# Kernel optimization log

Measured on AMD Instinct MI355X. Metric: run time of the kernel, lower is better.

Reference implementation:

```python
import jax, jax.numpy as jnp
import numpy as np

N = 50000      # total nodes across batched subgraphs
E = 800000     # total edges
R = 4          # num_relations
G = 16         # number of graphs (questions) in batch
NODE_DIM = 128
QDIM = 768
RQ = 64        # reduced_qn_dim
RN = 64        # reduced_node_dim
H = 128        # hidden_dim
OUT = 64       # output_dim


def setup_inputs() -> dict:
    key = jax.random.key(0)
    ks = jax.random.split(key, 16)
    def lin(k, i, o):
        return jax.random.normal(k, (i, o), jnp.float32) / np.float32(np.sqrt(i))
    def rel(k, i, o):
        return jax.random.normal(k, (R, i, o), jnp.float32) / np.float32(np.sqrt(i))
    return {
        "x": jax.random.normal(ks[0], (N, NODE_DIM), jnp.float32),
        "edge_index": jax.random.randint(ks[1], (2, E), 0, N, dtype=jnp.int32),
        "edge_attr": jax.random.randint(ks[2], (E,), 0, R, dtype=jnp.int32),
        "batch": jnp.sort(jax.random.randint(ks[3], (N,), 0, G, dtype=jnp.int32)),
        "question_embedding": jax.random.normal(ks[4], (G, QDIM), jnp.float32),
        "qn_W": lin(ks[5], QDIM, RQ), "qn_b": jnp.zeros((RQ,), jnp.float32),
        "W0": rel(ks[6], NODE_DIM, RN), "root0": lin(ks[7], NODE_DIM, RN), "b0": jnp.zeros((RN,), jnp.float32),
        "W1": rel(ks[8], RN + RQ, H), "root1": lin(ks[9], RN + RQ, H), "b1": jnp.zeros((H,), jnp.float32),
        "W2": rel(ks[10], H, H), "root2": lin(ks[11], H, H), "b2": jnp.zeros((H,), jnp.float32),
        "W3": rel(ks[12], H, OUT), "root3": lin(ks[13], H, OUT), "b3": jnp.zeros((OUT,), jnp.float32),
    }


def rgcn_conv(x, src, dst, etype, W, root, b):
    """PyG RGCNConv: out_i = x_i @ root + b + sum_r mean_{j in N_r(i)} x_j @ W_r."""
    out = x @ root + b
    for r in range(R):
        h = x @ W[r]                                  # [N, out] transform-then-gather
        mask = (etype == r)
        msgs = jnp.where(mask[:, None], h[src], 0.0)  # [E, out]
        s = jax.ops.segment_sum(msgs, dst, num_segments=N)
        cnt = jax.ops.segment_sum(mask.astype(x.dtype), dst, num_segments=N)
        out = out + s / jnp.maximum(cnt, 1.0)[:, None]
    return out


def reference(x, edge_index, edge_attr, batch, question_embedding,
              qn_W, qn_b, W0, root0, b0, W1, root1, b1, W2, root2, b2, W3, root3, b3):
    src, dst = edge_index[0], edge_index[1]
    q = jax.nn.relu(question_embedding @ qn_W + qn_b)          # [G, RQ]
    h = jax.nn.relu(rgcn_conv(x, src, dst, edge_attr, W0, root0, b0))
    combined = jnp.concatenate([h, q[batch]], axis=1)          # [N, RN+RQ]
    h = jax.nn.relu(rgcn_conv(combined, src, dst, edge_attr, W1, root1, b1))
    h = jax.nn.relu(rgcn_conv(h, src, dst, edge_attr, W2, root2, b2))
    return rgcn_conv(h, src, dst, edge_attr, W3, root3, b3)
```

## Files before the change

### kernel.cpp

```cpp
#include <hip/hip_runtime.h>
#include <hip/hip_bf16.h>

#define NN 50000
#define EE 800000
#define GG 16
#define QD 768
#define NBUCK 196
#define EPB 4000

typedef __bf16 bf16x8 __attribute__((ext_vector_type(8)));
typedef float f32x4 __attribute__((ext_vector_type(4)));

static __device__ __forceinline__ float bflo(unsigned u) {
    union { unsigned v; float f; } c; c.v = u << 16; return c.f;
}
static __device__ __forceinline__ float bfhi(unsigned u) {
    union { unsigned v; float f; } c; c.v = u & 0xffff0000u; return c.f;
}


__global__ void qkern(const float* __restrict__ qe, const float* __restrict__ W,
                      const float* __restrict__ b, float* __restrict__ q) {
    int g = blockIdx.x, o = threadIdx.x;
    float s = b[o];
    for (int k = 0; k < QD; ++k) s = fmaf(qe[g * QD + k], W[k * 64 + o], s);
    q[g * 64 + o] = fmaxf(s, 0.f);
}

__global__ void convert_x(const float* __restrict__ x, __hip_bfloat16* __restrict__ xb, int n4) {
    int i = blockIdx.x * blockDim.x + threadIdx.x;
    if (i >= n4) return;
    float4 v = ((const float4*)x)[i];
    union { ushort4 u; __hip_bfloat16 h[4]; } o;
    o.h[0] = __float2bfloat16(v.x); o.h[1] = __float2bfloat16(v.y);
    o.h[2] = __float2bfloat16(v.z); o.h[3] = __float2bfloat16(v.w);
    ((ushort4*)xb)[i] = o.u;
}

__global__ void prep_w(const float* __restrict__ W, const float* __restrict__ root,
                       __hip_bfloat16* __restrict__ WT, int O) {
    int idx = blockIdx.x * blockDim.x + threadIdx.x;
    int total = 5 * O * 128;
    if (idx >= total) return;
    int n = idx >> 7, k = idx & 127;
    float v;
    if (n < 4 * O) { int r = n / O, o = n - r * O; v = W[((size_t)r * 128 + k) * O + o]; }
    else           { int o = n - 4 * O;            v = root[(size_t)k * O + o]; }
    WT[idx] = __float2bfloat16(v);
}


__global__ void bucket_hist(const int* __restrict__ dst, int* __restrict__ bcnt) {
    __shared__ int h[NBUCK];
    int tid = threadIdx.x;
    for (int i = tid; i < NBUCK; i += 256) h[i] = 0;
    __syncthreads();
    for (int e = blockIdx.x * 256 + tid; e < EE; e += gridDim.x * 256)
        atomicAdd(&h[dst[e] >> 8], 1);
    __syncthreads();
    for (int i = tid; i < NBUCK; i += 256) if (h[i]) atomicAdd(&bcnt[i], h[i]);
}

__global__ void bucket_scan(const int* __restrict__ bcnt, int* __restrict__ bbase,
                            int* __restrict__ bcur) {
    __shared__ int wt[4];
    int tid = threadIdx.x, lane = tid & 63, w = tid >> 6;
    int v = (tid < NBUCK) ? bcnt[tid] : 0;
    int sc = v;
#pragma unroll
    for (int off = 1; off < 64; off <<= 1) {
        int t = __shfl_up(sc, off, 64);
        if (lane >= off) sc += t;
    }
    if (lane == 63) wt[w] = sc;
    __syncthreads();
    int wbase = 0;
    for (int ww = 0; ww < w; ++ww) wbase += wt[ww];
    int excl = wbase + sc - v;
    if (tid <= NBUCK) bbase[tid] = excl;
    if (tid < NBUCK) bcur[tid] = excl;
}

__global__ __launch_bounds__(256) void bin_edges(const int* __restrict__ src,
                                                 const int* __restrict__ dst,
                                                 const int* __restrict__ et,
                                                 int* __restrict__ bcur,
                                                 unsigned* __restrict__ binned) {
    __shared__ int lcnt[NBUCK];
    __shared__ int lbase[NBUCK];
    int tid = threadIdx.x;
    int e0 = blockIdx.x * EPB, e1 = min(e0 + EPB, EE);
    for (int base = e0; base < e1; base += 2048) {
        for (int i = tid; i < NBUCK; i += 256) lcnt[i] = 0;
        __syncthreads();
        unsigned ent[8]; int bk[8], rk[8];
#pragma unroll
        for (int k = 0; k < 8; ++k) {
            int e = base + k * 256 + tid;
            if (e < e1) {
                int d = dst[e];
                bk[k] = d >> 8;
                ent[k] = ((unsigned)src[e] << 10) | ((unsigned)et[e] << 8) | (unsigned)(d & 255);
                rk[k] = atomicAdd(&lcnt[bk[k]], 1);
            } else bk[k] = -1;
        }
        __syncthreads();
        for (int i = tid; i < NBUCK; i += 256)
            lbase[i] = lcnt[i] ? atomicAdd(&bcur[i], lcnt[i]) : 0;
        __syncthreads();
#pragma unroll
        for (int k = 0; k < 8; ++k)
            if (bk[k] >= 0) binned[lbase[bk[k]] + rk[k]] = ent[k];
        __syncthreads();
    }
}

__global__ __launch_bounds__(256) void csr_fine(const int* __restrict__ bbase,
                                                const unsigned* __restrict__ binned,
                                                int* __restrict__ csr,
                                                int* __restrict__ offsets,
                                                float* __restrict__ inv4) {
    __shared__ int cnt[1024];
    __shared__ int wt[4];
    int b = blockIdx.x, tid = threadIdx.x, lane = tid & 63, w = tid >> 6;
    int seg0 = bbase[b], seg1 = bbase[b + 1];
    for (int i = tid; i < 1024; i += 256) cnt[i] = 0;
    __syncthreads();
    for (int e = seg0 + tid; e < seg1; e += 256) {
        unsigned u = binned[e];
        atomicAdd(&cnt[(u & 255) * 4 + ((u >> 8) & 3)], 1);
    }
    __syncthreads();
    int c0 = cnt[tid * 4], c1 = cnt[tid * 4 + 1], c2 = cnt[tid * 4 + 2], c3 = cnt[tid * 4 + 3];
    int s = c0 + c1 + c2 + c3;
    int sc = s;
#pragma unroll
    for (int off = 1; off < 64; off <<= 1) {
        int t = __shfl_up(sc, off, 64);
        if (lane >= off) sc += t;
    }
    if (lane == 63) wt[w] = sc;
    __syncthreads();
    int wbase = 0;
    for (int ww = 0; ww < w; ++ww) wbase += wt[ww];
    int excl = wbase + sc - s;
    cnt[tid * 4]     = excl;
    cnt[tid * 4 + 1] = excl + c0;
    cnt[tid * 4 + 2] = excl + c0 + c1;
    cnt[tid * 4 + 3] = excl + c0 + c1 + c2;
    int node = b * 256 + tid;
    if (node < NN) {
        offsets[node] = seg0 + excl;
        float4 iv;
        iv.x = 1.f / fmaxf((float)c0, 1.f);
        iv.y = 1.f / fmaxf((float)c1, 1.f);
        iv.z = 1.f / fmaxf((float)c2, 1.f);
        iv.w = 1.f / fmaxf((float)c3, 1.f);
        ((float4*)inv4)[node] = iv;
    }
    if (b == NBUCK - 1 && tid == 0) offsets[NN] = EE;
    __syncthreads();
    for (int e = seg0 + tid; e < seg1; e += 256) {
        unsigned u = binned[e];
        int r = atomicAdd(&cnt[(u & 255) * 4 + ((u >> 8) & 3)], 1);
        csr[seg0 + r] = (int)(((u >> 10) << 2) | ((u >> 8) & 3));
    }
}


template <int O>
__global__ __launch_bounds__(256) void dense_mm(const __hip_bfloat16* __restrict__ X,
                                                const __hip_bfloat16* __restrict__ WT,
                                                __hip_bfloat16* __restrict__ hall_b,
                                                float* __restrict__ hroot) {
    __shared__ char tilebuf[4][4096];
    int wave = threadIdx.x >> 6;
    int lane = threadIdx.x & 63;
    int quad = lane >> 4, l15 = lane & 15;
    int cg = blockIdx.x;
    int slot = (O == 64) ? cg : (cg >> 1);
    int colbase = (O == 128 && (cg & 1)) ? 64 : 0;
    const __bf16* Xs = (const __bf16*)X;
    const __bf16* Ws = (const __bf16*)WT;

    bf16x8 b[4][4];
#pragma unroll
    for (int kk = 0; kk < 4; ++kk)
#pragma unroll
        for (int t = 0; t < 4; ++t)
            b[kk][t] = *(const bf16x8*)(Ws + (size_t)(cg * 64 + t * 16 + l15) * 128 + kk * 32 + quad * 8);

    int tile0 = blockIdx.y * 32 + wave * 8;
    for (int i = 0; i < 8; ++i) {
        int tile = tile0 + i;
        if (tile >= NN / 16) break;
        int m0 = tile * 16;

        bf16x8 a[4];
#pragma unroll
        for (int kk = 0; kk < 4; ++kk)
            a[kk] = *(const bf16x8*)(Xs + (size_t)(m0 + l15) * 128 + kk * 32 + quad * 8);

        f32x4 acc[4] = {f32x4{0,0,0,0}, f32x4{0,0,0,0}, f32x4{0,0,0,0}, f32x4{0,0,0,0}};
#pragma unroll
        for (int kk = 0; kk < 4; ++kk)
#pragma unroll
            for (int t = 0; t < 4; ++t)
                acc[t] = __builtin_amdgcn_mfma_f32_16x16x32_bf16(a[kk], b[kk][t], acc[t], 0, 0, 0);

        if (slot == 4) {
            float* tp = (float*)tilebuf[wave];
#pragma unroll
            for (int t = 0; t < 4; ++t)
#pragma unroll
                for (int reg = 0; reg < 4; ++reg)
                    tp[(quad * 4 + reg) * 64 + t * 16 + l15] = acc[t][reg];
#pragma unroll
            for (int p = 0; p < 4; ++p) {
                int c = p * 64 + lane;
                int row = c >> 4, col0 = (c & 15) * 4;
                *(f32x4*)&hroot[(size_t)(m0 + row) * O + colbase + col0] =
                    ((const f32x4*)tp)[c];
            }
        } else {
            __hip_bfloat16* tp = (__hip_bfloat16*)tilebuf[wave];
#pragma unroll
            for (int t = 0; t < 4; ++t)
#pragma unroll
                for (int reg = 0; reg < 4; ++reg)
                    tp[(quad * 4 + reg) * 64 + t * 16 + l15] = __float2bfloat16(acc[t][reg]);
#pragma unroll
            for (int p = 0; p < 2; ++p) {
                int c = p * 64 + lane;
                int row = c >> 3, col0 = (c & 7) * 8;
                *(uint4*)&hall_b[((size_t)(m0 + row) * 4 + slot) * O + colbase + col0] =
                    ((const uint4*)tp)[c];
            }
        }
    }
}


template <int O, int MODE>
__global__ __launch_bounds__(256) void aggregate(const __hip_bfloat16* __restrict__ hall_b,
                                                 const float* __restrict__ hroot,
                                                 const int* __restrict__ offsets,
                                                 const int* __restrict__ csr,
                                                 const float* __restrict__ inv4,
                                                 const float* __restrict__ bias,
                                                 const float* __restrict__ q,
                                                 const int* __restrict__ batch,
                                                 __hip_bfloat16* __restrict__ xnext,
                                                 float* __restrict__ out) {
    int node = blockIdx.x * 4 + (threadIdx.x >> 6);
    int lane = threadIdx.x & 63;
    int e0 = offsets[node], e1 = offsets[node + 1];
    float4 iv = ((const float4*)inv4)[node];
    float acc0 = 0.f, acc1 = 0.f;
    const char* hb = (const char*)hall_b;
    for (int base = e0; base < e1; base += 64) {
        int e = base + lane;
        int packed = (e < e1) ? csr[e] : 0;
        int m = min(64, e1 - base);
        int j = 0;
        for (; j + 4 <= m; j += 4) {
            int p0 = __builtin_amdgcn_readlane(packed, j);
            int p1 = __builtin_amdgcn_readlane(packed, j + 1);
            int p2 = __builtin_amdgcn_readlane(packed, j + 2);
            int p3 = __builtin_amdgcn_readlane(packed, j + 3);
            int r0 = p0 & 3, r1 = p1 & 3, r2 = p2 & 3, r3 = p3 & 3;
            float w0 = (r0 == 0) ? iv.x : (r0 == 1) ? iv.y : (r0 == 2) ? iv.z : iv.w;
            float w1 = (r1 == 0) ? iv.x : (r1 == 1) ? iv.y : (r1 == 2) ? iv.z : iv.w;
            float w2 = (r2 == 0) ? iv.x : (r2 == 1) ? iv.y : (r2 == 2) ? iv.z : iv.w;
            float w3 = (r3 == 0) ? iv.x : (r3 == 1) ? iv.y : (r3 == 2) ? iv.z : iv.w;
            if (O == 64) {
                unsigned u0 = *(const unsigned short*)(hb + (size_t)p0 * 128 + lane * 2);
                unsigned u1 = *(const unsigned short*)(hb + (size_t)p1 * 128 + lane * 2);
                unsigned u2 = *(const unsigned short*)(hb + (size_t)p2 * 128 + lane * 2);
                unsigned u3 = *(const unsigned short*)(hb + (size_t)p3 * 128 + lane * 2);
                acc0 = fmaf(w0, bflo(u0), acc0);
                acc0 = fmaf(w1, bflo(u1), acc0);
                acc0 = fmaf(w2, bflo(u2), acc0);
                acc0 = fmaf(w3, bflo(u3), acc0);
            } else {
                unsigned u0 = *(const unsigned*)(hb + (size_t)p0 * 256 + lane * 4);
                unsigned u1 = *(const unsigned*)(hb + (size_t)p1 * 256 + lane * 4);
                unsigned u2 = *(const unsigned*)(hb + (size_t)p2 * 256 + lane * 4);
                unsigned u3 = *(const unsigned*)(hb + (size_t)p3 * 256 + lane * 4);
                acc0 = fmaf(w0, bflo(u0), acc0);  acc1 = fmaf(w0, bfhi(u0), acc1);
                acc0 = fmaf(w1, bflo(u1), acc0);  acc1 = fmaf(w1, bfhi(u1), acc1);
                acc0 = fmaf(w2, bflo(u2), acc0);  acc1 = fmaf(w2, bfhi(u2), acc1);
                acc0 = fmaf(w3, bflo(u3), acc0);  acc1 = fmaf(w3, bfhi(u3), acc1);
            }
        }
        for (; j < m; ++j) {
            int p = __builtin_amdgcn_readlane(packed, j);
            int r = p & 3;
            float wgt = (r == 0) ? iv.x : (r == 1) ? iv.y : (r == 2) ? iv.z : iv.w;
            if (O == 64) {
                unsigned u = *(const unsigned short*)(hb + (size_t)p * 128 + lane * 2);
                acc0 = fmaf(wgt, bflo(u), acc0);
            } else {
                unsigned u = *(const unsigned*)(hb + (size_t)p * 256 + lane * 4);
                acc0 = fmaf(wgt, bflo(u), acc0);
                acc1 = fmaf(wgt, bfhi(u), acc1);
            }
        }
    }
    if (MODE == 0) {
        float v0 = hroot[(size_t)node * 64 + lane] + bias[lane] + acc0;
        xnext[(size_t)node * 128 + lane] = __float2bfloat16(fmaxf(v0, 0.f));
        float qv = q[batch[node] * 64 + lane];
        xnext[(size_t)node * 128 + 64 + lane] = __float2bfloat16(qv);
    } else if (MODE == 1) {
        float2 rr = *(const float2*)(hroot + (size_t)node * 128 + 2 * lane);
        float2 bb = *(const float2*)(bias + 2 * lane);
        float v0 = fmaxf(rr.x + bb.x + acc0, 0.f);
        float v1 = fmaxf(rr.y + bb.y + acc1, 0.f);
        __hip_bfloat16 h0 = __float2bfloat16(v0), h1 = __float2bfloat16(v1);
        ushort2 pk;
        pk.x = *(unsigned short*)&h0; pk.y = *(unsigned short*)&h1;
        ((ushort2*)xnext)[(size_t)node * 64 + lane] = pk;
    } else {
        out[(size_t)node * 64 + lane] = hroot[(size_t)node * 64 + lane] + bias[lane] + acc0;
    }
}


static inline size_t rup(size_t x) { return (x + 255) & ~(size_t)255; }

extern "C" void kernel_launch(void* const* d_in, const int* in_sizes, int n_in,
                              void* d_out, int out_size, void* d_ws, size_t ws_size,
                              hipStream_t stream) {
    const float* x      = (const float*)d_in[0];
    const int*   esrc   = (const int*)d_in[1];
    const int*   edst   = esrc + EE;
    const int*   eattr  = (const int*)d_in[2];
    const int*   batch  = (const int*)d_in[3];
    const float* qe     = (const float*)d_in[4];
    const float* qn_W   = (const float*)d_in[5];
    const float* qn_b   = (const float*)d_in[6];
    const float* W0 = (const float*)d_in[7],  *root0 = (const float*)d_in[8],  *b0 = (const float*)d_in[9];
    const float* W1 = (const float*)d_in[10], *root1 = (const float*)d_in[11], *b1 = (const float*)d_in[12];
    const float* W2 = (const float*)d_in[13], *root2 = (const float*)d_in[14], *b2 = (const float*)d_in[15];
    const float* W3 = (const float*)d_in[16], *root3 = (const float*)d_in[17], *b3 = (const float*)d_in[18];
    float* out = (float*)d_out;

    char* w = (char*)d_ws;
    float* q       = (float*)w;  w += rup(GG * 64 * 4);
    float* inv4    = (float*)w;  w += rup((size_t)NN * 4 * 4);
    int*   offsets = (int*)w;    w += rup(((size_t)NN + 1) * 4);
    int*   bcnt    = (int*)w;    w += rup((size_t)NBUCK * 4);
    int*   bbase   = (int*)w;    w += rup(((size_t)NBUCK + 1) * 4);
    int*   bcur    = (int*)w;    w += rup((size_t)NBUCK * 4);
    unsigned* binned = (unsigned*)w; w += rup((size_t)EE * 4);
    int*   csr     = (int*)w;    w += rup((size_t)EE * 4);
    __hip_bfloat16* WT0 = (__hip_bfloat16*)w; w += rup((size_t)5 * 64 * 128 * 2);
    __hip_bfloat16* WT1 = (__hip_bfloat16*)w; w += rup((size_t)5 * 128 * 128 * 2);
    __hip_bfloat16* WT2 = (__hip_bfloat16*)w; w += rup((size_t)5 * 128 * 128 * 2);
    __hip_bfloat16* WT3 = (__hip_bfloat16*)w; w += rup((size_t)5 * 64 * 128 * 2);
    __hip_bfloat16* xb0 = (__hip_bfloat16*)w; w += rup((size_t)NN * 128 * 2);
    __hip_bfloat16* xb1 = (__hip_bfloat16*)w; w += rup((size_t)NN * 128 * 2);
    __hip_bfloat16* hall_b = (__hip_bfloat16*)w; w += rup((size_t)NN * 4 * 128 * 2);
    float* hroot   = (float*)w;  w += rup((size_t)NN * 128 * 4);

    hipMemsetAsync(bcnt, 0, (size_t)NBUCK * 4, stream);

    qkern<<<GG, 64, 0, stream>>>(qe, qn_W, qn_b, q);
    convert_x<<<(NN * 128 / 4 + 255) / 256, 256, 0, stream>>>(x, xb0, NN * 128 / 4);
    prep_w<<<(5 * 64 * 128 + 255) / 256, 256, 0, stream>>>(W0, root0, WT0, 64);
    prep_w<<<(5 * 128 * 128 + 255) / 256, 256, 0, stream>>>(W1, root1, WT1, 128);
    prep_w<<<(5 * 128 * 128 + 255) / 256, 256, 0, stream>>>(W2, root2, WT2, 128);
    prep_w<<<(5 * 64 * 128 + 255) / 256, 256, 0, stream>>>(W3, root3, WT3, 64);

    bucket_hist<<<256, 256, 0, stream>>>(edst, bcnt);
    bucket_scan<<<1, 256, 0, stream>>>(bcnt, bbase, bcur);
    bin_edges<<<(EE + EPB - 1) / EPB, 256, 0, stream>>>(esrc, edst, eattr, bcur, binned);
    csr_fine<<<NBUCK, 256, 0, stream>>>(bbase, binned, csr, offsets, inv4);

    int rowgrp = (NN / 16 + 31) / 32;
    int aggblk = NN / 4;

    dense_mm<64><<<dim3(5, rowgrp), 256, 0, stream>>>(xb0, WT0, hall_b, hroot);
    aggregate<64, 0><<<aggblk, 256, 0, stream>>>(hall_b, hroot, offsets, csr, inv4, b0, q, batch, xb1, nullptr);

    dense_mm<128><<<dim3(10, rowgrp), 256, 0, stream>>>(xb1, WT1, hall_b, hroot);
    aggregate<128, 1><<<aggblk, 256, 0, stream>>>(hall_b, hroot, offsets, csr, inv4, b1, nullptr, nullptr, xb0, nullptr);

    dense_mm<128><<<dim3(10, rowgrp), 256, 0, stream>>>(xb0, WT2, hall_b, hroot);
    aggregate<128, 1><<<aggblk, 256, 0, stream>>>(hall_b, hroot, offsets, csr, inv4, b2, nullptr, nullptr, xb1, nullptr);

    dense_mm<64><<<dim3(5, rowgrp), 256, 0, stream>>>(xb1, WT3, hall_b, hroot);
    aggregate<64, 2><<<aggblk, 256, 0, stream>>>(hall_b, hroot, offsets, csr, inv4, b3, nullptr, nullptr, nullptr, out);
}
```

Baseline: 435.3 us.

## Aggregate raw features per relation before transform, then one fused K=640 GEMM

Reorders each RGCN layer from transform-then-gather to gather-then-transform. A new agg_x kernel computes per-relation mean-aggregated 128-wide bf16 inputs, concatenated with the self row into a 640-wide X5. A dense5 MFMA GEMM then multiplies X5 by stacked [root;W0..W3] weights and fuses bias, ReLU, the q concat and the output write. This removes the 4x-wide hall_b intermediate and the fp32 hroot buffer, and gathers only 256 bytes per edge. In exchange it writes and reads a 640-wide X5 per layer, and it rounds the aggregated means to bf16 before the transform, which changes numerics.

```diff
diff --git a/kernel.cpp b/kernel.cpp
--- a/kernel.cpp
+++ b/kernel.cpp
@@ -37,16 +37,15 @@
     ((ushort4*)xb)[i] = o.u;
 }
 
-__global__ void prep_w(const float* __restrict__ W, const float* __restrict__ root,
-                       __hip_bfloat16* __restrict__ WT, int O) {
+__global__ void prep_w5(const float* __restrict__ W, const float* __restrict__ root,
+                        __hip_bfloat16* __restrict__ W5T, int O) {
     int idx = blockIdx.x * blockDim.x + threadIdx.x;
-    int total = 5 * O * 128;
-    if (idx >= total) return;
-    int n = idx >> 7, k = idx & 127;
+    if (idx >= O * 640) return;
+    int o = idx / 640, k = idx - o * 640;
     float v;
-    if (n < 4 * O) { int r = n / O, o = n - r * O; v = W[((size_t)r * 128 + k) * O + o]; }
-    else           { int o = n - 4 * O;            v = root[(size_t)k * O + o]; }
-    WT[idx] = __float2bfloat16(v);
+    if (k < 128) v = root[(size_t)k * O + o];
+    else { int r = (k - 128) >> 7, kk = (k - 128) & 127; v = W[((size_t)r * 128 + kk) * O + o]; }
+    W5T[idx] = __float2bfloat16(v);
 }
 
 
@@ -119,7 +118,7 @@
                                                 const unsigned* __restrict__ binned,
                                                 int* __restrict__ csr,
                                                 int* __restrict__ offsets,
-                                                float* __restrict__ inv4) {
+                                                int4* __restrict__ cnt4) {
     __shared__ int cnt[1024];
     __shared__ int wt[4];
     int b = blockIdx.x, tid = threadIdx.x, lane = tid & 63, w = tid >> 6;
@@ -151,12 +150,7 @@
     int node = b * 256 + tid;
     if (node < NN) {
         offsets[node] = seg0 + excl;
-        float4 iv;
-        iv.x = 1.f / fmaxf((float)c0, 1.f);
-        iv.y = 1.f / fmaxf((float)c1, 1.f);
-        iv.z = 1.f / fmaxf((float)c2, 1.f);
-        iv.w = 1.f / fmaxf((float)c3, 1.f);
-        ((float4*)inv4)[node] = iv;
+        cnt4[node] = make_int4(c0, c1, c2, c3);
     }
     if (b == NBUCK - 1 && tid == 0) offsets[NN] = EE;
     __syncthreads();
@@ -168,161 +162,166 @@
 }
 
 
-template <int O>
-__global__ __launch_bounds__(256) void dense_mm(const __hip_bfloat16* __restrict__ X,
-                                                const __hip_bfloat16* __restrict__ WT,
-                                                __hip_bfloat16* __restrict__ hall_b,
-                                                float* __restrict__ hroot) {
-    __shared__ char tilebuf[4][4096];
-    int wave = threadIdx.x >> 6;
-    int lane = threadIdx.x & 63;
-    int quad = lane >> 4, l15 = lane & 15;
-    int cg = blockIdx.x;
-    int slot = (O == 64) ? cg : (cg >> 1);
-    int colbase = (O == 128 && (cg & 1)) ? 64 : 0;
-    const __bf16* Xs = (const __bf16*)X;
-    const __bf16* Ws = (const __bf16*)WT;
-
-    bf16x8 b[4][4];
-#pragma unroll
-    for (int kk = 0; kk < 4; ++kk)
-#pragma unroll
-        for (int t = 0; t < 4; ++t)
-            b[kk][t] = *(const bf16x8*)(Ws + (size_t)(cg * 64 + t * 16 + l15) * 128 + kk * 32 + quad * 8);
-
-    int tile0 = blockIdx.y * 32 + wave * 8;
-    for (int i = 0; i < 8; ++i) {
-        int tile = tile0 + i;
-        if (tile >= NN / 16) break;
-        int m0 = tile * 16;
-
-        bf16x8 a[4];
-#pragma unroll
-        for (int kk = 0; kk < 4; ++kk)
-            a[kk] = *(const bf16x8*)(Xs + (size_t)(m0 + l15) * 128 + kk * 32 + quad * 8);
-
-        f32x4 acc[4] = {f32x4{0,0,0,0}, f32x4{0,0,0,0}, f32x4{0,0,0,0}, f32x4{0,0,0,0}};
-#pragma unroll
-        for (int kk = 0; kk < 4; ++kk)
-#pragma unroll
-            for (int t = 0; t < 4; ++t)
-                acc[t] = __builtin_amdgcn_mfma_f32_16x16x32_bf16(a[kk], b[kk][t], acc[t], 0, 0, 0);
-
-        if (slot == 4) {
-            float* tp = (float*)tilebuf[wave];
-#pragma unroll
-            for (int t = 0; t < 4; ++t)
-#pragma unroll
-                for (int reg = 0; reg < 4; ++reg)
-                    tp[(quad * 4 + reg) * 64 + t * 16 + l15] = acc[t][reg];
-#pragma unroll
-            for (int p = 0; p < 4; ++p) {
-                int c = p * 64 + lane;
-                int row = c >> 4, col0 = (c & 15) * 4;
-                *(f32x4*)&hroot[(size_t)(m0 + row) * O + colbase + col0] =
-                    ((const f32x4*)tp)[c];
-            }
-        } else {
-            __hip_bfloat16* tp = (__hip_bfloat16*)tilebuf[wave];
-#pragma unroll
-            for (int t = 0; t < 4; ++t)
-#pragma unroll
-                for (int reg = 0; reg < 4; ++reg)
-                    tp[(quad * 4 + reg) * 64 + t * 16 + l15] = __float2bfloat16(acc[t][reg]);
-#pragma unroll
-            for (int p = 0; p < 2; ++p) {
-                int c = p * 64 + lane;
-                int row = c >> 3, col0 = (c & 7) * 8;
-                *(uint4*)&hall_b[((size_t)(m0 + row) * 4 + slot) * O + colbase + col0] =
-                    ((const uint4*)tp)[c];
-            }
-        }
-    }
-}
-
-
-template <int O, int MODE>
-__global__ __launch_bounds__(256) void aggregate(const __hip_bfloat16* __restrict__ hall_b,
-                                                 const float* __restrict__ hroot,
-                                                 const int* __restrict__ offsets,
-                                                 const int* __restrict__ csr,
-                                                 const float* __restrict__ inv4,
-                                                 const float* __restrict__ bias,
-                                                 const float* __restrict__ q,
-                                                 const int* __restrict__ batch,
-                                                 __hip_bfloat16* __restrict__ xnext,
-                                                 float* __restrict__ out) {
+__global__ __launch_bounds__(256) void agg_x(const __hip_bfloat16* __restrict__ X,
+                                             const int* __restrict__ offsets,
+                                             const int4* __restrict__ cnt4,
+                                             const int* __restrict__ csr,
+                                             __hip_bfloat16* __restrict__ X5) {
     int node = blockIdx.x * 4 + (threadIdx.x >> 6);
     int lane = threadIdx.x & 63;
-    int e0 = offsets[node], e1 = offsets[node + 1];
-    float4 iv = ((const float4*)inv4)[node];
-    float acc0 = 0.f, acc1 = 0.f;
-    const char* hb = (const char*)hall_b;
-    for (int base = e0; base < e1; base += 64) {
-        int e = base + lane;
-        int packed = (e < e1) ? csr[e] : 0;
-        int m = min(64, e1 - base);
-        int j = 0;
-        for (; j + 4 <= m; j += 4) {
-            int p0 = __builtin_amdgcn_readlane(packed, j);
-            int p1 = __builtin_amdgcn_readlane(packed, j + 1);
-            int p2 = __builtin_amdgcn_readlane(packed, j + 2);
-            int p3 = __builtin_amdgcn_readlane(packed, j + 3);
-            int r0 = p0 & 3, r1 = p1 & 3, r2 = p2 & 3, r3 = p3 & 3;
-            float w0 = (r0 == 0) ? iv.x : (r0 == 1) ? iv.y : (r0 == 2) ? iv.z : iv.w;
-            float w1 = (r1 == 0) ? iv.x : (r1 == 1) ? iv.y : (r1 == 2) ? iv.z : iv.w;
-            float w2 = (r2 == 0) ? iv.x : (r2 == 1) ? iv.y : (r2 == 2) ? iv.z : iv.w;
-            float w3 = (r3 == 0) ? iv.x : (r3 == 1) ? iv.y : (r3 == 2) ? iv.z : iv.w;
-            if (O == 64) {
-                unsigned u0 = *(const unsigned short*)(hb + (size_t)p0 * 128 + lane * 2);
-                unsigned u1 = *(const unsigned short*)(hb + (size_t)p1 * 128 + lane * 2);
-                unsigned u2 = *(const unsigned short*)(hb + (size_t)p2 * 128 + lane * 2);
-                unsigned u3 = *(const unsigned short*)(hb + (size_t)p3 * 128 + lane * 2);
-                acc0 = fmaf(w0, bflo(u0), acc0);
-                acc0 = fmaf(w1, bflo(u1), acc0);
-                acc0 = fmaf(w2, bflo(u2), acc0);
-                acc0 = fmaf(w3, bflo(u3), acc0);
-            } else {
-                unsigned u0 = *(const unsigned*)(hb + (size_t)p0 * 256 + lane * 4);
-                unsigned u1 = *(const unsigned*)(hb + (size_t)p1 * 256 + lane * 4);
-                unsigned u2 = *(const unsigned*)(hb + (size_t)p2 * 256 + lane * 4);
-                unsigned u3 = *(const unsigned*)(hb + (size_t)p3 * 256 + lane * 4);
-                acc0 = fmaf(w0, bflo(u0), acc0);  acc1 = fmaf(w0, bfhi(u0), acc1);
-                acc0 = fmaf(w1, bflo(u1), acc0);  acc1 = fmaf(w1, bfhi(u1), acc1);
-                acc0 = fmaf(w2, bflo(u2), acc0);  acc1 = fmaf(w2, bfhi(u2), acc1);
-                acc0 = fmaf(w3, bflo(u3), acc0);  acc1 = fmaf(w3, bfhi(u3), acc1);
-            }
-        }
-        for (; j < m; ++j) {
-            int p = __builtin_amdgcn_readlane(packed, j);
-            int r = p & 3;
-            float wgt = (r == 0) ? iv.x : (r == 1) ? iv.y : (r == 2) ? iv.z : iv.w;
-            if (O == 64) {
-                unsigned u = *(const unsigned short*)(hb + (size_t)p * 128 + lane * 2);
-                acc0 = fmaf(wgt, bflo(u), acc0);
-            } else {
-                unsigned u = *(const unsigned*)(hb + (size_t)p * 256 + lane * 4);
-                acc0 = fmaf(wgt, bflo(u), acc0);
-                acc1 = fmaf(wgt, bfhi(u), acc1);
-            }
-        }
-    }
-    if (MODE == 0) {
-        float v0 = hroot[(size_t)node * 64 + lane] + bias[lane] + acc0;
-        xnext[(size_t)node * 128 + lane] = __float2bfloat16(fmaxf(v0, 0.f));
-        float qv = q[batch[node] * 64 + lane];
-        xnext[(size_t)node * 128 + 64 + lane] = __float2bfloat16(qv);
-    } else if (MODE == 1) {
-        float2 rr = *(const float2*)(hroot + (size_t)node * 128 + 2 * lane);
-        float2 bb = *(const float2*)(bias + 2 * lane);
-        float v0 = fmaxf(rr.x + bb.x + acc0, 0.f);
-        float v1 = fmaxf(rr.y + bb.y + acc1, 0.f);
-        __hip_bfloat16 h0 = __float2bfloat16(v0), h1 = __float2bfloat16(v1);
+    const char* xb = (const char*)X;
+    char* x5 = (char*)X5;
+    unsigned self = *(const unsigned*)(xb + (size_t)node * 256 + lane * 4);
+    *(unsigned*)(x5 + (size_t)node * 1280 + lane * 4) = self;
+    int e = offsets[node];
+    int4 c4 = cnt4[node];
+#pragma unroll
+    for (int r = 0; r < 4; ++r) {
+        int cr = (r == 0) ? c4.x : (r == 1) ? c4.y : (r == 2) ? c4.z : c4.w;
+        float acc0 = 0.f, acc1 = 0.f;
+        for (int base = 0; base < cr; base += 64) {
+            int i = base + lane;
+            int packed = (i < cr) ? csr[e + i] : 0;
+            int m = min(64, cr - base);
+            int j = 0;
+            for (; j + 4 <= m; j += 4) {
+                int p0 = __builtin_amdgcn_readlane(packed, j)     >> 2;
+                int p1 = __builtin_amdgcn_readlane(packed, j + 1) >> 2;
+                int p2 = __builtin_amdgcn_readlane(packed, j + 2) >> 2;
+                int p3 = __builtin_amdgcn_readlane(packed, j + 3) >> 2;
+                unsigned u0 = *(const unsigned*)(xb + (size_t)p0 * 256 + lane * 4);
+                unsigned u1 = *(const unsigned*)(xb + (size_t)p1 * 256 + lane * 4);
+                unsigned u2 = *(const unsigned*)(xb + (size_t)p2 * 256 + lane * 4);
+                unsigned u3 = *(const unsigned*)(xb + (size_t)p3 * 256 + lane * 4);
+                acc0 += bflo(u0); acc1 += bfhi(u0);
+                acc0 += bflo(u1); acc1 += bfhi(u1);
+                acc0 += bflo(u2); acc1 += bfhi(u2);
+                acc0 += bflo(u3); acc1 += bfhi(u3);
+            }
+            for (; j < m; ++j) {
+                int p = __builtin_amdgcn_readlane(packed, j) >> 2;
+                unsigned u = *(const unsigned*)(xb + (size_t)p * 256 + lane * 4);
+                acc0 += bflo(u); acc1 += bfhi(u);
+            }
+        }
+        e += cr;
+        float inv = 1.f / fmaxf((float)cr, 1.f);
+        __hip_bfloat16 h0 = __float2bfloat16(acc0 * inv), h1 = __float2bfloat16(acc1 * inv);
         ushort2 pk;
         pk.x = *(unsigned short*)&h0; pk.y = *(unsigned short*)&h1;
-        ((ushort2*)xnext)[(size_t)node * 64 + lane] = pk;
-    } else {
-        out[(size_t)node * 64 + lane] = hroot[(size_t)node * 64 + lane] + bias[lane] + acc0;
+        *(ushort2*)(x5 + (size_t)node * 1280 + 256 + r * 256 + lane * 4) = pk;
+    }
+}
+
+
+template <int O, int MODE>
+__global__ __launch_bounds__(256) void dense5(const __hip_bfloat16* __restrict__ X5,
+                                              const __hip_bfloat16* __restrict__ W5T,
+                                              const float* __restrict__ bias,
+                                              const float* __restrict__ q,
+                                              const int* __restrict__ batch,
+                                              __hip_bfloat16* __restrict__ xnext,
+                                              float* __restrict__ out) {
+    __shared__ char lds[16384];
+    constexpr int NCT = O / 16;
+    int tid = threadIdx.x;
+    int wave = tid >> 6, lane = tid & 63;
+    int quad = lane >> 4, l15 = lane & 15;
+    int mbase = blockIdx.x * 128 + wave * 32;
+    const __bf16* Xs = (const __bf16*)X5;
+    const __bf16* Ws = (const __bf16*)W5T;
+
+    f32x4 acc[2][NCT];
+#pragma unroll
+    for (int mt = 0; mt < 2; ++mt)
+#pragma unroll
+        for (int t = 0; t < NCT; ++t) acc[mt][t] = f32x4{0, 0, 0, 0};
+
+    int arow0 = min(mbase + l15, NN - 1);
+    int arow1 = min(mbase + 16 + l15, NN - 1);
+    const __bf16* ap0 = Xs + (size_t)arow0 * 640;
+    const __bf16* ap1 = Xs + (size_t)arow1 * 640;
+
+    for (int kc = 0; kc < 10; ++kc) {
+        int k0 = kc * 64;
+        __syncthreads();
+        constexpr int NF = NCT * 2 * 64;
+#pragma unroll
+        for (int i = 0; i < NF / 256; ++i) {
+            int f = tid + i * 256;
+            int fl = f & 63;
+            int o = (f >> 7) * 16 + (fl & 15);
+            int kk = k0 + ((f >> 6) & 1) * 32 + ((fl >> 4) & 3) * 8;
+            *(uint4*)(lds + f * 16) = *(const uint4*)(Ws + (size_t)o * 640 + kk);
+        }
+        __syncthreads();
+#pragma unroll
+        for (int ks = 0; ks < 2; ++ks) {
+            bf16x8 a0 = *(const bf16x8*)(ap0 + k0 + ks * 32 + quad * 8);
+            bf16x8 a1 = *(const bf16x8*)(ap1 + k0 + ks * 32 + quad * 8);
+#pragma unroll
+            for (int t = 0; t < NCT; ++t) {
+                bf16x8 b = *(const bf16x8*)(lds + ((t * 2 + ks) * 64 + lane) * 16);
+                acc[0][t] = __builtin_amdgcn_mfma_f32_16x16x32_bf16(a0, b, acc[0][t], 0, 0, 0);
+                acc[1][t] = __builtin_amdgcn_mfma_f32_16x16x32_bf16(a1, b, acc[1][t], 0, 0, 0);
+            }
+        }
+    }
+    __syncthreads();
+
+    if (MODE == 2) {
+#pragma unroll
+        for (int mt = 0; mt < 2; ++mt)
+#pragma unroll
+            for (int t = 0; t < NCT; ++t) {
+                int col = t * 16 + l15;
+                float bv = bias[col];
+#pragma unroll
+                for (int reg = 0; reg < 4; ++reg) {
+                    int row = mbase + mt * 16 + quad * 4 + reg;
+                    if (row < NN) out[(size_t)row * 64 + col] = acc[mt][t][reg] + bv;
+                }
+            }
+        return;
+    }
+
+    __hip_bfloat16* tp = (__hip_bfloat16*)(lds + wave * 4096);
+#pragma unroll
+    for (int mt = 0; mt < 2; ++mt) {
+        int m0 = mbase + mt * 16;
+#pragma unroll
+        for (int t = 0; t < NCT; ++t) {
+            int col = t * 16 + l15;
+            float bv = bias[col];
+#pragma unroll
+            for (int reg = 0; reg < 4; ++reg)
+                tp[(quad * 4 + reg) * 128 + col] =
+                    __float2bfloat16(fmaxf(acc[mt][t][reg] + bv, 0.f));
+        }
+        if (MODE == 0) {
+            int row = lane >> 2;
+            int cs = (lane & 3) * 16;
+            int rnode = min(m0 + row, NN - 1);
+            int g = batch[rnode];
+#pragma unroll
+            for (int i = 0; i < 4; ++i) {
+                float4 v = *(const float4*)(q + g * 64 + cs + i * 4);
+                __hip_bfloat16 h0 = __float2bfloat16(v.x), h1 = __float2bfloat16(v.y);
+                __hip_bfloat16 h2 = __float2bfloat16(v.z), h3 = __float2bfloat16(v.w);
+                ushort4 pk;
+                pk.x = *(unsigned short*)&h0; pk.y = *(unsigned short*)&h1;
+                pk.z = *(unsigned short*)&h2; pk.w = *(unsigned short*)&h3;
+                *(ushort4*)(tp + row * 128 + 64 + cs + i * 4) = pk;
+            }
+        }
+#pragma unroll
+        for (int p = 0; p < 4; ++p) {
+            int c = p * 64 + lane;
+            int row = m0 + (c >> 4);
+            if (row < NN)
+                *(uint4*)((char*)xnext + (size_t)row * 256 + (c & 15) * 16) =
+                    *(const uint4*)((const char*)tp + c * 16);
+        }
     }
 }
 
@@ -348,48 +347,47 @@
 
     char* w = (char*)d_ws;
     float* q       = (float*)w;  w += rup(GG * 64 * 4);
-    float* inv4    = (float*)w;  w += rup((size_t)NN * 4 * 4);
     int*   offsets = (int*)w;    w += rup(((size_t)NN + 1) * 4);
+    int4*  cnt4    = (int4*)w;   w += rup((size_t)NN * 16);
     int*   bcnt    = (int*)w;    w += rup((size_t)NBUCK * 4);
     int*   bbase   = (int*)w;    w += rup(((size_t)NBUCK + 1) * 4);
     int*   bcur    = (int*)w;    w += rup((size_t)NBUCK * 4);
     unsigned* binned = (unsigned*)w; w += rup((size_t)EE * 4);
     int*   csr     = (int*)w;    w += rup((size_t)EE * 4);
-    __hip_bfloat16* WT0 = (__hip_bfloat16*)w; w += rup((size_t)5 * 64 * 128 * 2);
-    __hip_bfloat16* WT1 = (__hip_bfloat16*)w; w += rup((size_t)5 * 128 * 128 * 2);
-    __hip_bfloat16* WT2 = (__hip_bfloat16*)w; w += rup((size_t)5 * 128 * 128 * 2);
-    __hip_bfloat16* WT3 = (__hip_bfloat16*)w; w += rup((size_t)5 * 64 * 128 * 2);
-    __hip_bfloat16* xb0 = (__hip_bfloat16*)w; w += rup((size_t)NN * 128 * 2);
-    __hip_bfloat16* xb1 = (__hip_bfloat16*)w; w += rup((size_t)NN * 128 * 2);
-    __hip_bfloat16* hall_b = (__hip_bfloat16*)w; w += rup((size_t)NN * 4 * 128 * 2);
-    float* hroot   = (float*)w;  w += rup((size_t)NN * 128 * 4);
+    __hip_bfloat16* W5T0 = (__hip_bfloat16*)w; w += rup((size_t)64 * 640 * 2);
+    __hip_bfloat16* W5T1 = (__hip_bfloat16*)w; w += rup((size_t)128 * 640 * 2);
+    __hip_bfloat16* W5T2 = (__hip_bfloat16*)w; w += rup((size_t)128 * 640 * 2);
+    __hip_bfloat16* W5T3 = (__hip_bfloat16*)w; w += rup((size_t)64 * 640 * 2);
+    __hip_bfloat16* xb0 = (__hip_bfloat16*)w;  w += rup((size_t)NN * 128 * 2);
+    __hip_bfloat16* xb1 = (__hip_bfloat16*)w;  w += rup((size_t)NN * 128 * 2);
+    __hip_bfloat16* X5  = (__hip_bfloat16*)w;  w += rup((size_t)NN * 640 * 2);
 
     hipMemsetAsync(bcnt, 0, (size_t)NBUCK * 4, stream);
 
     qkern<<<GG, 64, 0, stream>>>(qe, qn_W, qn_b, q);
     convert_x<<<(NN * 128 / 4 + 255) / 256, 256, 0, stream>>>(x, xb0, NN * 128 / 4);
-    prep_w<<<(5 * 64 * 128 + 255) / 256, 256, 0, stream>>>(W0, root0, WT0, 64);
-    prep_w<<<(5 * 128 * 128 + 255) / 256, 256, 0, stream>>>(W1, root1, WT1, 128);
-    prep_w<<<(5 * 128 * 128 + 255) / 256, 256, 0, stream>>>(W2, root2, WT2, 128);
-    prep_w<<<(5 * 64 * 128 + 255) / 256, 256, 0, stream>>>(W3, root3, WT3, 64);
+    prep_w5<<<(64 * 640 + 255) / 256, 256, 0, stream>>>(W0, root0, W5T0, 64);
+    prep_w5<<<(128 * 640 + 255) / 256, 256, 0, stream>>>(W1, root1, W5T1, 128);
+    prep_w5<<<(128 * 640 + 255) / 256, 256, 0, stream>>>(W2, root2, W5T2, 128);
+    prep_w5<<<(64 * 640 + 255) / 256, 256, 0, stream>>>(W3, root3, W5T3, 64);
 
     bucket_hist<<<256, 256, 0, stream>>>(edst, bcnt);
     bucket_scan<<<1, 256, 0, stream>>>(bcnt, bbase, bcur);
     bin_edges<<<(EE + EPB - 1) / EPB, 256, 0, stream>>>(esrc, edst, eattr, bcur, binned);
-    csr_fine<<<NBUCK, 256, 0, stream>>>(bbase, binned, csr, offsets, inv4);
-
-    int rowgrp = (NN / 16 + 31) / 32;
+    csr_fine<<<NBUCK, 256, 0, stream>>>(bbase, binned, csr, offsets, cnt4);
+
     int aggblk = NN / 4;
-
-    dense_mm<64><<<dim3(5, rowgrp), 256, 0, stream>>>(xb0, WT0, hall_b, hroot);
-    aggregate<64, 0><<<aggblk, 256, 0, stream>>>(hall_b, hroot, offsets, csr, inv4, b0, q, batch, xb1, nullptr);
-
-    dense_mm<128><<<dim3(10, rowgrp), 256, 0, stream>>>(xb1, WT1, hall_b, hroot);
-    aggregate<128, 1><<<aggblk, 256, 0, stream>>>(hall_b, hroot, offsets, csr, inv4, b1, nullptr, nullptr, xb0, nullptr);
-
-    dense_mm<128><<<dim3(10, rowgrp), 256, 0, stream>>>(xb0, WT2, hall_b, hroot);
-    aggregate<128, 1><<<aggblk, 256, 0, stream>>>(hall_b, hroot, offsets, csr, inv4, b2, nullptr, nullptr, xb1, nullptr);
-
-    dense_mm<64><<<dim3(5, rowgrp), 256, 0, stream>>>(xb1, WT3, hall_b, hroot);
-    aggregate<64, 2><<<aggblk, 256, 0, stream>>>(hall_b, hroot, offsets, csr, inv4, b3, nullptr, nullptr, nullptr, out);
-}
+    int dblk = (NN + 127) / 128;
+
+    agg_x<<<aggblk, 256, 0, stream>>>(xb0, offsets, cnt4, csr, X5);
+    dense5<64, 0><<<dblk, 256, 0, stream>>>(X5, W5T0, b0, q, batch, xb1, nullptr);
+
+    agg_x<<<aggblk, 256, 0, stream>>>(xb1, offsets, cnt4, csr, X5);
+    dense5<128, 1><<<dblk, 256, 0, stream>>>(X5, W5T1, b1, nullptr, nullptr, xb0, nullptr);
+
+    agg_x<<<aggblk, 256, 0, stream>>>(xb0, offsets, cnt4, csr, X5);
+    dense5<128, 1><<<dblk, 256, 0, stream>>>(X5, W5T2, b2, nullptr, nullptr, xb1, nullptr);
+
+    agg_x<<<aggblk, 256, 0, stream>>>(xb1, offsets, cnt4, csr, X5);
+    dense5<64, 2><<<dblk, 256, 0, stream>>>(X5, W5T3, b3, nullptr, nullptr, nullptr, out);
+}
```

New measurement: 474.6 us. 1.09x slower.
